# Performance work log

Measured on AMD Instinct MI355X. Metric: run time of the kernel, lower is better.

## Reference

```python
import jax, jax.numpy as jnp
import numpy as np
from jax import lax

S, B, IN, H, L = 256, 8192, 1, 32, 2


def setup_inputs() -> dict:
    key = jax.random.key(0)
    ks = jax.random.split(key, 12)
    s = 1.0 / np.sqrt(H)
    return {
        "x": jax.random.normal(ks[0], (S, B, IN), dtype=jnp.float32),
        "h": jax.random.normal(ks[1], (L, B, H), dtype=jnp.float32),
        "W_ih0": jax.random.uniform(ks[2], (3 * H, IN), jnp.float32, -s, s),
        "W_hh0": jax.random.uniform(ks[3], (3 * H, H), jnp.float32, -s, s),
        "b_ih0": jax.random.uniform(ks[4], (3 * H,), jnp.float32, -s, s),
        "b_hh0": jax.random.uniform(ks[5], (3 * H,), jnp.float32, -s, s),
        "W_ih1": jax.random.uniform(ks[6], (3 * H, H), jnp.float32, -s, s),
        "W_hh1": jax.random.uniform(ks[7], (3 * H, H), jnp.float32, -s, s),
        "b_ih1": jax.random.uniform(ks[8], (3 * H,), jnp.float32, -s, s),
        "b_hh1": jax.random.uniform(ks[9], (3 * H,), jnp.float32, -s, s),
        "W_out": jax.random.uniform(ks[10], (1, H), jnp.float32, -s, s),
        "b_out": jax.random.uniform(ks[11], (1,), jnp.float32, -s, s),
    }


def _gru_layer(x_seq, h0, W_ih, W_hh, b_ih, b_hh):
    # x_seq: (S, B, D_in), h0: (B, H). PyTorch GRU gate math.
    def step(h, x_t):
        gi = x_t @ W_ih.T + b_ih            # (B, 3H)
        gh = h @ W_hh.T + b_hh              # (B, 3H)
        i_r, i_z, i_n = jnp.split(gi, 3, axis=-1)
        h_r, h_z, h_n = jnp.split(gh, 3, axis=-1)
        r = jax.nn.sigmoid(i_r + h_r)
        z = jax.nn.sigmoid(i_z + h_z)
        n = jnp.tanh(i_n + r * h_n)
        h_new = (1.0 - z) * n + z * h
        return h_new, h_new

    h_last, out = lax.scan(step, h0, x_seq)
    return out, h_last


def reference(x, h, W_ih0, W_hh0, b_ih0, b_hh0, W_ih1, W_hh1, b_ih1, b_hh1, W_out, b_out):
    out0, hl0 = _gru_layer(x, h[0], W_ih0, W_hh0, b_ih0, b_hh0)
    out1, hl1 = _gru_layer(out0, h[1], W_ih1, W_hh1, b_ih1, b_hh1)
    # per-timestep Linear loop == one batched matmul over (S, B, H)
    y = out1 @ W_out.T + b_out              # (S, B, 1)
    h_state = jnp.stack([hl0, hl1], axis=0)  # (L, B, H)
    return (y, h_state)
```

## Files before the change

kernel.cpp:

```cpp
#include <hip/hip_runtime.h>


#define S_LEN 256
#define B_SZ  8192
#define H_SZ  32
#define RS    40

typedef __attribute__((ext_vector_type(8))) short short8;
typedef __attribute__((ext_vector_type(4))) float f32x4;

#define MFMA(a, b, c) __builtin_amdgcn_mfma_f32_16x16x32_bf16(a, b, c, 0, 0, 0)

#if __has_builtin(__builtin_amdgcn_exp2f)
#define EXP2F(x) __builtin_amdgcn_exp2f(x)
#else
#define EXP2F(x) exp2f(x)
#endif
#if __has_builtin(__builtin_amdgcn_rcpf)
#define RCPF(x) __builtin_amdgcn_rcpf(x)
#else
#define RCPF(x) (1.0f / (x))
#endif

__device__ __forceinline__ float sigm_pre(float p) {
    return RCPF(1.0f + EXP2F(p));
}
__device__ __forceinline__ float tanh_pre(float p) {
    return 1.0f - 2.0f * RCPF(1.0f + EXP2F(p));
}

__device__ __forceinline__ unsigned short bf_rne1(float f) {
    union { float f; unsigned u; } x; x.f = f;
    unsigned u = x.u + 0x7fffu + ((x.u >> 16) & 1u);
    return (unsigned short)(u >> 16);
}

#if __has_builtin(__builtin_amdgcn_cvt_pk_bf16_f32)
typedef __bf16 bf16x2 __attribute__((ext_vector_type(2)));
__device__ __forceinline__ unsigned pk2(float a, float b) {
    union { bf16x2 v; unsigned u; } c;
    c.v = __builtin_amdgcn_cvt_pk_bf16_f32(a, b);
    return c.u;
}
#else
__device__ __forceinline__ unsigned pk2(float a, float b) {
    return (unsigned)bf_rne1(a) | ((unsigned)bf_rne1(b) << 16);
}
#endif

union Frag { short8 s8; unsigned u[4]; };

__global__ __launch_bounds__(256) void gru_bf(
    const float* __restrict__ x,
    const float* __restrict__ h_in,
    const float* __restrict__ W_ih0,
    const float* __restrict__ W_hh0,
    const float* __restrict__ b_ih0,
    const float* __restrict__ b_hh0,
    const float* __restrict__ W_ih1,
    const float* __restrict__ W_hh1,
    const float* __restrict__ b_ih1,
    const float* __restrict__ b_hh1,
    const float* __restrict__ W_out,
    const float* __restrict__ b_out,
    float* __restrict__ out)
{
    __shared__ __align__(16) float sx[S_LEN * 16];
    __shared__ __align__(16) float sy[2][S_LEN * 16];
    __shared__ __align__(16) unsigned short sh0s[3][16 * RS];
    __shared__ __align__(16) unsigned short sh1s[3][16 * RS];

    const int tid  = threadIdx.x;
    const int w    = tid >> 6;
    const int lane = tid & 63;
    const int n    = lane & 15;
    const int q    = lane >> 4;
    const int base = blockIdx.x * 16;
    const int bn   = base + n;
    const int wl   = w & 1;

    for (int s = tid; s < S_LEN * 4; s += 256) {
        const int t = s >> 2, c = s & 3;
        *(float4*)&sx[t * 16 + c * 4] = *(const float4*)&x[t * B_SZ + base + c * 4];
    }

    const float SRZ = -1.4426950408889634f;
    const float SN  =  2.8853900817779268f;

    short8 A_h[3], A_i[3];
    f32x4  C_h[3], C_i3;
    float  wi0r[4], wi0z[4], wi0n[4], bi0n[4];
    float  wo[4];
    float  hd[4];

    if (w < 2) {
#pragma unroll
        for (int t = 0; t < 3; ++t) {
            const float sc = (t < 2) ? SRZ : SN;
            const int row = 32 * t + 16 * wl + n;
#pragma unroll
            for (int e = 0; e < 8; ++e)
                A_h[t][e] = (short)bf_rne1(W_hh0[row * H_SZ + q * 8 + e] * sc);
#pragma unroll
            for (int r = 0; r < 4; ++r) {
                const int g = 32 * t + 16 * wl + 4 * q + r;
                C_h[t][r] = (t < 2) ? SRZ * (b_ih0[g] + b_hh0[g])
                                    : SN * b_hh0[g];
            }
        }
#pragma unroll
        for (int r = 0; r < 4; ++r) {
            const int j = 16 * wl + 4 * q + r;
            wi0r[r] = SRZ * W_ih0[j];
            wi0z[r] = SRZ * W_ih0[32 + j];
            wi0n[r] = SN  * W_ih0[64 + j];
            bi0n[r] = SN  * b_ih0[64 + j];
            hd[r]   = h_in[bn * H_SZ + j];
            wo[r]   = 0.f;
        }
    } else {
#pragma unroll
        for (int t = 0; t < 3; ++t) {
            const float sc = (t < 2) ? SRZ : SN;
            const int row = 32 * t + 16 * wl + n;
#pragma unroll
            for (int e = 0; e < 8; ++e) {
                A_h[t][e] = (short)bf_rne1(W_hh1[row * H_SZ + q * 8 + e] * sc);
                A_i[t][e] = (short)bf_rne1(W_ih1[row * H_SZ + q * 8 + e] * sc);
            }
#pragma unroll
            for (int r = 0; r < 4; ++r) {
                const int g = 32 * t + 16 * wl + 4 * q + r;
                C_h[t][r] = (t < 2) ? SRZ * (b_ih1[g] + b_hh1[g])
                                    : SN * b_hh1[g];
                if (t == 2) C_i3[r] = SN * b_ih1[g];
            }
        }
#pragma unroll
        for (int r = 0; r < 4; ++r) {
            const int j = 16 * wl + 4 * q + r;
            hd[r] = h_in[B_SZ * H_SZ + bn * H_SZ + j];
            wo[r] = W_out[j];
        }
    }
    const f32x4 Z4 = {0.f, 0.f, 0.f, 0.f};
    const float bout = b_out[0];

    short8 B0, B1;
    {
        Frag f;
        const float4 a = *(const float4*)&h_in[bn * H_SZ + q * 8];
        const float4 b = *(const float4*)&h_in[bn * H_SZ + q * 8 + 4];
        f.u[0] = pk2(a.x, a.y); f.u[1] = pk2(a.z, a.w);
        f.u[2] = pk2(b.x, b.y); f.u[3] = pk2(b.z, b.w);
        B0 = f.s8;
        const float4 c = *(const float4*)&h_in[B_SZ * H_SZ + bn * H_SZ + q * 8];
        const float4 d = *(const float4*)&h_in[B_SZ * H_SZ + bn * H_SZ + q * 8 + 4];
        f.u[0] = pk2(c.x, c.y); f.u[1] = pk2(c.z, c.w);
        f.u[2] = pk2(d.x, d.y); f.u[3] = pk2(d.z, d.w);
        B1 = f.s8;
    }

    __syncthreads();

    int buf = 0;
#pragma unroll 1
    for (int i = 0; i <= S_LEN; ++i) {
        if (w < 2) {
            if (i < S_LEN) {
                const float xc = sx[i * 16 + n];
                const f32x4 g0r = MFMA(A_h[0], B0, C_h[0]);
                const f32x4 g0z = MFMA(A_h[1], B0, C_h[1]);
                const f32x4 g0n = MFMA(A_h[2], B0, C_h[2]);
                float hv4[4];
#pragma unroll
                for (int r = 0; r < 4; ++r) {
                    const float rg = sigm_pre(fmaf(xc, wi0r[r], g0r[r]));
                    const float zg = sigm_pre(fmaf(xc, wi0z[r], g0z[r]));
                    const float ng = tanh_pre(fmaf(rg, g0n[r],
                                                   fmaf(xc, wi0n[r], bi0n[r])));
                    const float hv = fmaf(zg, hd[r] - ng, ng);
                    hd[r] = hv;
                    hv4[r] = hv;
                }
                *(uint2*)&sh0s[buf][n * RS + 16 * wl + 4 * q] =
                    make_uint2(pk2(hv4[0], hv4[1]), pk2(hv4[2], hv4[3]));
            }
        } else {
            if (i > 0) {
                const f32x4 ur = MFMA(A_h[0], B1, C_h[0]);
                const f32x4 uz = MFMA(A_h[1], B1, C_h[1]);
                const f32x4 un = MFMA(A_h[2], B1, C_h[2]);
                const f32x4 vr = MFMA(A_i[0], B0, Z4);
                const f32x4 vz = MFMA(A_i[1], B0, Z4);
                const f32x4 vn = MFMA(A_i[2], B0, C_i3);
                float hv4[4];
                float ys = 0.f;
#pragma unroll
                for (int r = 0; r < 4; ++r) {
                    const float rg = sigm_pre(ur[r] + vr[r]);
                    const float zg = sigm_pre(uz[r] + vz[r]);
                    const float ng = tanh_pre(fmaf(rg, un[r], vn[r]));
                    const float hv = fmaf(zg, hd[r] - ng, ng);
                    hd[r] = hv;
                    hv4[r] = hv;
                    ys = fmaf(hv, wo[r], ys);
                }
                *(uint2*)&sh1s[buf][n * RS + 16 * wl + 4 * q] =
                    make_uint2(pk2(hv4[0], hv4[1]), pk2(hv4[2], hv4[3]));
                ys += __shfl_xor(ys, 16);
                ys += __shfl_xor(ys, 32);
                if (lane < 16) sy[wl][(i - 1) * 16 + n] = ys;
            }
        }

        __syncthreads();

        if (i < S_LEN)
            B0 = *(const short8*)&sh0s[buf][n * RS + q * 8];
        if (w >= 2 && i > 0)
            B1 = *(const short8*)&sh1s[buf][n * RS + q * 8];

        buf = (buf == 2) ? 0 : buf + 1;
    }

    __syncthreads();

    for (int s = tid; s < S_LEN * 4; s += 256) {
        const int t = s >> 2, c = s & 3;
        const float4 a = *(const float4*)&sy[0][t * 16 + c * 4];
        const float4 b = *(const float4*)&sy[1][t * 16 + c * 4];
        *(float4*)&out[t * B_SZ + base + c * 4] =
            make_float4(a.x + b.x + bout, a.y + b.y + bout,
                        a.z + b.z + bout, a.w + b.w + bout);
    }

    const int j = 16 * wl + 4 * q;
    if (w < 2)
        *(float4*)&out[S_LEN * B_SZ + bn * H_SZ + j] =
            make_float4(hd[0], hd[1], hd[2], hd[3]);
    else
        *(float4*)&out[S_LEN * B_SZ + B_SZ * H_SZ + bn * H_SZ + j] =
            make_float4(hd[0], hd[1], hd[2], hd[3]);
}

extern "C" void kernel_launch(void* const* d_in, const int* in_sizes, int n_in,
                              void* d_out, int out_size, void* d_ws, size_t ws_size,
                              hipStream_t stream) {
    (void)in_sizes; (void)n_in; (void)out_size; (void)d_ws; (void)ws_size;
    const float* x     = (const float*)d_in[0];
    const float* h_in  = (const float*)d_in[1];
    const float* W_ih0 = (const float*)d_in[2];
    const float* W_hh0 = (const float*)d_in[3];
    const float* b_ih0 = (const float*)d_in[4];
    const float* b_hh0 = (const float*)d_in[5];
    const float* W_ih1 = (const float*)d_in[6];
    const float* W_hh1 = (const float*)d_in[7];
    const float* b_ih1 = (const float*)d_in[8];
    const float* b_hh1 = (const float*)d_in[9];
    const float* W_out = (const float*)d_in[10];
    const float* b_out = (const float*)d_in[11];

    dim3 grid(B_SZ / 16);
    dim3 block(256);
    gru_bf<<<grid, block, 0, stream>>>(x, h_in, W_ih0, W_hh0, b_ih0, b_hh0,
                                       W_ih1, W_hh1, b_ih1, b_hh1,
                                       W_out, b_out, (float*)d_out);
}
```

Baseline: 269.0 us.

## Process two 16-column batch groups per wave for ILP in the GRU recurrence

Each block now handles 32 batch columns, and every wave runs two independent 16-column groups through the MFMA and gate math. This halves the grid and interleaves two dependency chains to hide MFMA and transcendental latency in the serial time loop. The output projection moves from the layer-1 waves to the otherwise lighter layer-0 waves, read back from shared memory, and the hidden-state ring buffer drops from three slots to two. x is now stored as bf16 in shared memory, which adds rounding error on the layer-0 input. Register pressure also rises with doubled accumulators and state.

```diff
diff --git a/kernel.cpp b/kernel.cpp
--- a/kernel.cpp
+++ b/kernel.cpp
@@ -48,9 +48,11 @@
 }
 #endif
 
-union Frag { short8 s8; unsigned u[4]; };
-
-__global__ __launch_bounds__(256) void gru_bf(
+__device__ __forceinline__ float bits_f(unsigned u) {
+    union { unsigned u; float f; } x; x.u = u; return x.f;
+}
+
+__global__ __launch_bounds__(256) void gru_ilp2(
     const float* __restrict__ x,
     const float* __restrict__ h_in,
     const float* __restrict__ W_ih0,
@@ -65,23 +67,24 @@
     const float* __restrict__ b_out,
     float* __restrict__ out)
 {
-    __shared__ __align__(16) float sx[S_LEN * 16];
-    __shared__ __align__(16) float sy[2][S_LEN * 16];
-    __shared__ __align__(16) unsigned short sh0s[3][16 * RS];
-    __shared__ __align__(16) unsigned short sh1s[3][16 * RS];
+    __shared__ __align__(16) unsigned short sxs[S_LEN * 32];
+    __shared__ __align__(16) float sy[S_LEN * 32];
+    __shared__ __align__(16) unsigned short sh0s[2][32 * RS];
+    __shared__ __align__(16) unsigned short sh1s[2][32 * RS];
 
     const int tid  = threadIdx.x;
     const int w    = tid >> 6;
     const int lane = tid & 63;
     const int n    = lane & 15;
     const int q    = lane >> 4;
-    const int base = blockIdx.x * 16;
-    const int bn   = base + n;
+    const int base = blockIdx.x * 32;
     const int wl   = w & 1;
 
-    for (int s = tid; s < S_LEN * 4; s += 256) {
-        const int t = s >> 2, c = s & 3;
-        *(float4*)&sx[t * 16 + c * 4] = *(const float4*)&x[t * B_SZ + base + c * 4];
+    for (int s = tid; s < S_LEN * 8; s += 256) {
+        const int t = s >> 3, c = s & 7;
+        const float4 v = *(const float4*)&x[t * B_SZ + base + c * 4];
+        *(uint2*)&sxs[t * 32 + c * 4] =
+            make_uint2(pk2(v.x, v.y), pk2(v.z, v.w));
     }
 
     const float SRZ = -1.4426950408889634f;
@@ -90,8 +93,8 @@
     short8 A_h[3], A_i[3];
     f32x4  C_h[3], C_i3;
     float  wi0r[4], wi0z[4], wi0n[4], bi0n[4];
-    float  wo[4];
-    float  hd[4];
+    float  wo8[8];
+    float  hd[2][4];
 
     if (w < 2) {
 #pragma unroll
@@ -115,9 +118,14 @@
             wi0z[r] = SRZ * W_ih0[32 + j];
             wi0n[r] = SN  * W_ih0[64 + j];
             bi0n[r] = SN  * b_ih0[64 + j];
-            hd[r]   = h_in[bn * H_SZ + j];
-            wo[r]   = 0.f;
-        }
+        }
+#pragma unroll
+        for (int e = 0; e < 8; ++e) wo8[e] = W_out[q * 8 + e];
+#pragma unroll
+        for (int g = 0; g < 2; ++g)
+#pragma unroll
+            for (int r = 0; r < 4; ++r)
+                hd[g][r] = h_in[(base + g * 16 + n) * H_SZ + 16 * wl + 4 * q + r];
     } else {
 #pragma unroll
         for (int t = 0; t < 3; ++t) {
@@ -137,111 +145,150 @@
             }
         }
 #pragma unroll
-        for (int r = 0; r < 4; ++r) {
-            const int j = 16 * wl + 4 * q + r;
-            hd[r] = h_in[B_SZ * H_SZ + bn * H_SZ + j];
-            wo[r] = W_out[j];
-        }
+        for (int g = 0; g < 2; ++g)
+#pragma unroll
+            for (int r = 0; r < 4; ++r)
+                hd[g][r] = h_in[B_SZ * H_SZ +
+                                (base + g * 16 + n) * H_SZ + 16 * wl + 4 * q + r];
     }
     const f32x4 Z4 = {0.f, 0.f, 0.f, 0.f};
     const float bout = b_out[0];
 
-    short8 B0, B1;
-    {
-        Frag f;
-        const float4 a = *(const float4*)&h_in[bn * H_SZ + q * 8];
-        const float4 b = *(const float4*)&h_in[bn * H_SZ + q * 8 + 4];
+    short8 B0[2], B1[2];
+#pragma unroll
+    for (int g = 0; g < 2; ++g) {
+        const int bg = base + g * 16 + n;
+        union { short8 s8; unsigned u[4]; } f;
+        float4 a = *(const float4*)&h_in[bg * H_SZ + q * 8];
+        float4 b = *(const float4*)&h_in[bg * H_SZ + q * 8 + 4];
         f.u[0] = pk2(a.x, a.y); f.u[1] = pk2(a.z, a.w);
         f.u[2] = pk2(b.x, b.y); f.u[3] = pk2(b.z, b.w);
-        B0 = f.s8;
-        const float4 c = *(const float4*)&h_in[B_SZ * H_SZ + bn * H_SZ + q * 8];
-        const float4 d = *(const float4*)&h_in[B_SZ * H_SZ + bn * H_SZ + q * 8 + 4];
-        f.u[0] = pk2(c.x, c.y); f.u[1] = pk2(c.z, c.w);
-        f.u[2] = pk2(d.x, d.y); f.u[3] = pk2(d.z, d.w);
-        B1 = f.s8;
+        B0[g] = f.s8;
+        a = *(const float4*)&h_in[B_SZ * H_SZ + bg * H_SZ + q * 8];
+        b = *(const float4*)&h_in[B_SZ * H_SZ + bg * H_SZ + q * 8 + 4];
+        f.u[0] = pk2(a.x, a.y); f.u[1] = pk2(a.z, a.w);
+        f.u[2] = pk2(b.x, b.y); f.u[3] = pk2(b.z, b.w);
+        B1[g] = f.s8;
     }
 
     __syncthreads();
 
-    int buf = 0;
 #pragma unroll 1
     for (int i = 0; i <= S_LEN; ++i) {
+        const int buf = i & 1;
         if (w < 2) {
             if (i < S_LEN) {
-                const float xc = sx[i * 16 + n];
-                const f32x4 g0r = MFMA(A_h[0], B0, C_h[0]);
-                const f32x4 g0z = MFMA(A_h[1], B0, C_h[1]);
-                const f32x4 g0n = MFMA(A_h[2], B0, C_h[2]);
-                float hv4[4];
-#pragma unroll
-                for (int r = 0; r < 4; ++r) {
-                    const float rg = sigm_pre(fmaf(xc, wi0r[r], g0r[r]));
-                    const float zg = sigm_pre(fmaf(xc, wi0z[r], g0z[r]));
-                    const float ng = tanh_pre(fmaf(rg, g0n[r],
-                                                   fmaf(xc, wi0n[r], bi0n[r])));
-                    const float hv = fmaf(zg, hd[r] - ng, ng);
-                    hd[r] = hv;
-                    hv4[r] = hv;
+                const f32x4 g0r = MFMA(A_h[0], B0[0], C_h[0]);
+                const f32x4 g0z = MFMA(A_h[1], B0[0], C_h[1]);
+                const f32x4 g0n = MFMA(A_h[2], B0[0], C_h[2]);
+                const f32x4 g1r = MFMA(A_h[0], B0[1], C_h[0]);
+                const f32x4 g1z = MFMA(A_h[1], B0[1], C_h[1]);
+                const f32x4 g1n = MFMA(A_h[2], B0[1], C_h[2]);
+                const float xc0 = bits_f((unsigned)sxs[i * 32 + n] << 16);
+                const float xc1 = bits_f((unsigned)sxs[i * 32 + 16 + n] << 16);
+#pragma unroll
+                for (int g = 0; g < 2; ++g) {
+                    const float xc = g ? xc1 : xc0;
+                    float hv4[4];
+#pragma unroll
+                    for (int r = 0; r < 4; ++r) {
+                        const float gr = g ? g1r[r] : g0r[r];
+                        const float gz = g ? g1z[r] : g0z[r];
+                        const float gn = g ? g1n[r] : g0n[r];
+                        const float rg = sigm_pre(fmaf(xc, wi0r[r], gr));
+                        const float zg = sigm_pre(fmaf(xc, wi0z[r], gz));
+                        const float ng = tanh_pre(fmaf(rg, gn,
+                                                       fmaf(xc, wi0n[r], bi0n[r])));
+                        const float hv = fmaf(zg, hd[g][r] - ng, ng);
+                        hd[g][r] = hv;
+                        hv4[r] = hv;
+                    }
+                    *(uint2*)&sh0s[buf][(g * 16 + n) * RS + 16 * wl + 4 * q] =
+                        make_uint2(pk2(hv4[0], hv4[1]), pk2(hv4[2], hv4[3]));
                 }
-                *(uint2*)&sh0s[buf][n * RS + 16 * wl + 4 * q] =
-                    make_uint2(pk2(hv4[0], hv4[1]), pk2(hv4[2], hv4[3]));
             }
         } else {
             if (i > 0) {
-                const f32x4 ur = MFMA(A_h[0], B1, C_h[0]);
-                const f32x4 uz = MFMA(A_h[1], B1, C_h[1]);
-                const f32x4 un = MFMA(A_h[2], B1, C_h[2]);
-                const f32x4 vr = MFMA(A_i[0], B0, Z4);
-                const f32x4 vz = MFMA(A_i[1], B0, Z4);
-                const f32x4 vn = MFMA(A_i[2], B0, C_i3);
-                float hv4[4];
-                float ys = 0.f;
-#pragma unroll
-                for (int r = 0; r < 4; ++r) {
-                    const float rg = sigm_pre(ur[r] + vr[r]);
-                    const float zg = sigm_pre(uz[r] + vz[r]);
-                    const float ng = tanh_pre(fmaf(rg, un[r], vn[r]));
-                    const float hv = fmaf(zg, hd[r] - ng, ng);
-                    hd[r] = hv;
-                    hv4[r] = hv;
-                    ys = fmaf(hv, wo[r], ys);
+                const f32x4 u0r = MFMA(A_h[0], B1[0], C_h[0]);
+                const f32x4 u0z = MFMA(A_h[1], B1[0], C_h[1]);
+                const f32x4 u0n = MFMA(A_h[2], B1[0], C_h[2]);
+                const f32x4 v0r = MFMA(A_i[0], B0[0], Z4);
+                const f32x4 v0z = MFMA(A_i[1], B0[0], Z4);
+                const f32x4 v0n = MFMA(A_i[2], B0[0], C_i3);
+                const f32x4 u1r = MFMA(A_h[0], B1[1], C_h[0]);
+                const f32x4 u1z = MFMA(A_h[1], B1[1], C_h[1]);
+                const f32x4 u1n = MFMA(A_h[2], B1[1], C_h[2]);
+                const f32x4 v1r = MFMA(A_i[0], B0[1], Z4);
+                const f32x4 v1z = MFMA(A_i[1], B0[1], Z4);
+                const f32x4 v1n = MFMA(A_i[2], B0[1], C_i3);
+#pragma unroll
+                for (int g = 0; g < 2; ++g) {
+                    float hv4[4];
+#pragma unroll
+                    for (int r = 0; r < 4; ++r) {
+                        const float ar = g ? u1r[r] + v1r[r] : u0r[r] + v0r[r];
+                        const float az = g ? u1z[r] + v1z[r] : u0z[r] + v0z[r];
+                        const float an = g ? u1n[r] : u0n[r];
+                        const float bn_ = g ? v1n[r] : v0n[r];
+                        const float rg = sigm_pre(ar);
+                        const float zg = sigm_pre(az);
+                        const float ng = tanh_pre(fmaf(rg, an, bn_));
+                        const float hv = fmaf(zg, hd[g][r] - ng, ng);
+                        hd[g][r] = hv;
+                        hv4[r] = hv;
+                    }
+                    *(uint2*)&sh1s[buf][(g * 16 + n) * RS + 16 * wl + 4 * q] =
+                        make_uint2(pk2(hv4[0], hv4[1]), pk2(hv4[2], hv4[3]));
                 }
-                *(uint2*)&sh1s[buf][n * RS + 16 * wl + 4 * q] =
-                    make_uint2(pk2(hv4[0], hv4[1]), pk2(hv4[2], hv4[3]));
-                ys += __shfl_xor(ys, 16);
-                ys += __shfl_xor(ys, 32);
-                if (lane < 16) sy[wl][(i - 1) * 16 + n] = ys;
             }
         }
 
         __syncthreads();
 
-        if (i < S_LEN)
-            B0 = *(const short8*)&sh0s[buf][n * RS + q * 8];
-        if (w >= 2 && i > 0)
-            B1 = *(const short8*)&sh1s[buf][n * RS + q * 8];
-
-        buf = (buf == 2) ? 0 : buf + 1;
+        if (i < S_LEN) {
+            B0[0] = *(const short8*)&sh0s[buf][n * RS + q * 8];
+            B0[1] = *(const short8*)&sh0s[buf][(16 + n) * RS + q * 8];
+            if (w >= 2 && i > 0) {
+                B1[0] = *(const short8*)&sh1s[buf][n * RS + q * 8];
+                B1[1] = *(const short8*)&sh1s[buf][(16 + n) * RS + q * 8];
+            }
+        }
+        if (w < 2 && i > 0) {
+            const uint4 d = *(const uint4*)&sh1s[buf][(wl * 16 + n) * RS + q * 8];
+            float ys =       bits_f(d.x << 16) * wo8[0];
+            ys = fmaf(bits_f(d.x & 0xffff0000u), wo8[1], ys);
+            ys = fmaf(bits_f(d.y << 16),         wo8[2], ys);
+            ys = fmaf(bits_f(d.y & 0xffff0000u), wo8[3], ys);
+            ys = fmaf(bits_f(d.z << 16),         wo8[4], ys);
+            ys = fmaf(bits_f(d.z & 0xffff0000u), wo8[5], ys);
+            ys = fmaf(bits_f(d.w << 16),         wo8[6], ys);
+            ys = fmaf(bits_f(d.w & 0xffff0000u), wo8[7], ys);
+            ys += __shfl_xor(ys, 16);
+            ys += __shfl_xor(ys, 32);
+            if (lane < 16) sy[(i - 1) * 32 + wl * 16 + n] = ys;
+        }
     }
 
     __syncthreads();
 
-    for (int s = tid; s < S_LEN * 4; s += 256) {
-        const int t = s >> 2, c = s & 3;
-        const float4 a = *(const float4*)&sy[0][t * 16 + c * 4];
-        const float4 b = *(const float4*)&sy[1][t * 16 + c * 4];
+    for (int s = tid; s < S_LEN * 8; s += 256) {
+        const int t = s >> 3, c = s & 7;
+        const float4 a = *(const float4*)&sy[t * 32 + c * 4];
         *(float4*)&out[t * B_SZ + base + c * 4] =
-            make_float4(a.x + b.x + bout, a.y + b.y + bout,
-                        a.z + b.z + bout, a.w + b.w + bout);
+            make_float4(a.x + bout, a.y + bout, a.z + bout, a.w + bout);
     }
 
     const int j = 16 * wl + 4 * q;
-    if (w < 2)
-        *(float4*)&out[S_LEN * B_SZ + bn * H_SZ + j] =
-            make_float4(hd[0], hd[1], hd[2], hd[3]);
-    else
-        *(float4*)&out[S_LEN * B_SZ + B_SZ * H_SZ + bn * H_SZ + j] =
-            make_float4(hd[0], hd[1], hd[2], hd[3]);
+#pragma unroll
+    for (int g = 0; g < 2; ++g) {
+        const int bg = base + g * 16 + n;
+        if (w < 2)
+            *(float4*)&out[S_LEN * B_SZ + bg * H_SZ + j] =
+                make_float4(hd[g][0], hd[g][1], hd[g][2], hd[g][3]);
+        else
+            *(float4*)&out[S_LEN * B_SZ + B_SZ * H_SZ + bg * H_SZ + j] =
+                make_float4(hd[g][0], hd[g][1], hd[g][2], hd[g][3]);
+    }
 }
 
 extern "C" void kernel_launch(void* const* d_in, const int* in_sizes, int n_in,
@@ -261,9 +308,9 @@
     const float* W_out = (const float*)d_in[10];
     const float* b_out = (const float*)d_in[11];
 
-    dim3 grid(B_SZ / 16);
+    dim3 grid(B_SZ / 32);
     dim3 block(256);
-    gru_bf<<<grid, block, 0, stream>>>(x, h_in, W_ih0, W_hh0, b_ih0, b_hh0,
-                                       W_ih1, W_hh1, b_ih1, b_hh1,
-                                       W_out, b_out, (float*)d_out);
-}
+    gru_ilp2<<<grid, block, 0, stream>>>(x, h_in, W_ih0, W_hh0, b_ih0, b_hh0,
+                                         W_ih1, W_hh1, b_ih1, b_hh1,
+                                         W_out, b_out, (float*)d_out);
+}
```

Result: slower. 289.7 us (+7.7%).

## Give each GRU layer a single wave and pipeline layers through an LDS ring

Applied to the files above, without the earlier changes.

Each layer's whole 32-wide hidden state now lives in one wavefront, so the per-step recurrence needs no block barrier. Layer 0 runs ahead in segments of 8 timesteps and writes its hidden states into a 16-slot LDS ring. Layer 1 consumes the previous segment and does its own recurrence through a private LDS transpose buffer, which cuts block-wide barriers from one per step to one per segment. The cost is twice the MFMA and activation work per wave, fewer waves per block (128 threads), and serialized latency inside each wave.

```diff
diff --git a/kernel.cpp b/kernel.cpp
--- a/kernel.cpp
+++ b/kernel.cpp
@@ -5,6 +5,8 @@
 #define B_SZ  8192
 #define H_SZ  32
 #define RS    40
+#define SEG   8
+#define NSLOT 16
 
 typedef __attribute__((ext_vector_type(8))) short short8;
 typedef __attribute__((ext_vector_type(4))) float f32x4;
@@ -48,9 +50,7 @@
 }
 #endif
 
-union Frag { short8 s8; unsigned u[4]; };
-
-__global__ __launch_bounds__(256) void gru_bf(
+__global__ __launch_bounds__(128, 1) void gru_auto(
     const float* __restrict__ x,
     const float* __restrict__ h_in,
     const float* __restrict__ W_ih0,
@@ -65,10 +65,10 @@
     const float* __restrict__ b_out,
     float* __restrict__ out)
 {
+    __shared__ __align__(16) unsigned short ring[NSLOT][16 * RS];
+    __shared__ __align__(16) unsigned short tr1[16 * RS];
     __shared__ __align__(16) float sx[S_LEN * 16];
-    __shared__ __align__(16) float sy[2][S_LEN * 16];
-    __shared__ __align__(16) unsigned short sh0s[3][16 * RS];
-    __shared__ __align__(16) unsigned short sh1s[3][16 * RS];
+    __shared__ __align__(16) float sy[S_LEN * 16];
 
     const int tid  = threadIdx.x;
     const int w    = tid >> 6;
@@ -77,9 +77,8 @@
     const int q    = lane >> 4;
     const int base = blockIdx.x * 16;
     const int bn   = base + n;
-    const int wl   = w & 1;
-
-    for (int s = tid; s < S_LEN * 4; s += 256) {
+
+    for (int s = tid; s < S_LEN * 4; s += 128) {
         const int t = s >> 2, c = s & 3;
         *(float4*)&sx[t * 16 + c * 4] = *(const float4*)&x[t * B_SZ + base + c * 4];
     }
@@ -87,161 +86,175 @@
     const float SRZ = -1.4426950408889634f;
     const float SN  =  2.8853900817779268f;
 
-    short8 A_h[3], A_i[3];
-    f32x4  C_h[3], C_i3;
-    float  wi0r[4], wi0z[4], wi0n[4], bi0n[4];
-    float  wo[4];
-    float  hd[4];
-
-    if (w < 2) {
-#pragma unroll
-        for (int t = 0; t < 3; ++t) {
-            const float sc = (t < 2) ? SRZ : SN;
-            const int row = 32 * t + 16 * wl + n;
+    short8 Am[6], Aa[6];
+    f32x4  Cm[6], Ca[2];
+    float  wir[2][4], wiz[2][4], win[2][4], bin[2][4];
+    float  wo[2][4];
+    float  hd[2][4];
+    short8 B0, B1, B0n;
+
+    if (w == 0) {
+#pragma unroll
+        for (int T = 0; T < 6; ++T) {
+            const float sc = (T < 4) ? SRZ : SN;
+            const int row = 16 * T + n;
 #pragma unroll
             for (int e = 0; e < 8; ++e)
-                A_h[t][e] = (short)bf_rne1(W_hh0[row * H_SZ + q * 8 + e] * sc);
-#pragma unroll
-            for (int r = 0; r < 4; ++r) {
-                const int g = 32 * t + 16 * wl + 4 * q + r;
-                C_h[t][r] = (t < 2) ? SRZ * (b_ih0[g] + b_hh0[g])
-                                    : SN * b_hh0[g];
+                Am[T][e] = (short)bf_rne1(W_hh0[row * H_SZ + q * 8 + e] * sc);
+#pragma unroll
+            for (int r = 0; r < 4; ++r) {
+                const int g = 16 * T + 4 * q + r;
+                Cm[T][r] = (T < 4) ? SRZ * (b_ih0[g] + b_hh0[g])
+                                   : SN * b_hh0[g];
             }
         }
 #pragma unroll
-        for (int r = 0; r < 4; ++r) {
-            const int j = 16 * wl + 4 * q + r;
-            wi0r[r] = SRZ * W_ih0[j];
-            wi0z[r] = SRZ * W_ih0[32 + j];
-            wi0n[r] = SN  * W_ih0[64 + j];
-            bi0n[r] = SN  * b_ih0[64 + j];
-            hd[r]   = h_in[bn * H_SZ + j];
-            wo[r]   = 0.f;
-        }
-    } else {
-#pragma unroll
-        for (int t = 0; t < 3; ++t) {
-            const float sc = (t < 2) ? SRZ : SN;
-            const int row = 32 * t + 16 * wl + n;
-#pragma unroll
-            for (int e = 0; e < 8; ++e) {
-                A_h[t][e] = (short)bf_rne1(W_hh1[row * H_SZ + q * 8 + e] * sc);
-                A_i[t][e] = (short)bf_rne1(W_ih1[row * H_SZ + q * 8 + e] * sc);
-            }
-#pragma unroll
-            for (int r = 0; r < 4; ++r) {
-                const int g = 32 * t + 16 * wl + 4 * q + r;
-                C_h[t][r] = (t < 2) ? SRZ * (b_ih1[g] + b_hh1[g])
-                                    : SN * b_hh1[g];
-                if (t == 2) C_i3[r] = SN * b_ih1[g];
-            }
-        }
-#pragma unroll
-        for (int r = 0; r < 4; ++r) {
-            const int j = 16 * wl + 4 * q + r;
-            hd[r] = h_in[B_SZ * H_SZ + bn * H_SZ + j];
-            wo[r] = W_out[j];
-        }
-    }
-    const f32x4 Z4 = {0.f, 0.f, 0.f, 0.f};
-    const float bout = b_out[0];
-
-    short8 B0, B1;
-    {
-        Frag f;
+        for (int h = 0; h < 2; ++h)
+#pragma unroll
+            for (int r = 0; r < 4; ++r) {
+                const int j = 16 * h + 4 * q + r;
+                wir[h][r] = SRZ * W_ih0[j];
+                wiz[h][r] = SRZ * W_ih0[32 + j];
+                win[h][r] = SN  * W_ih0[64 + j];
+                bin[h][r] = SN  * b_ih0[64 + j];
+                hd[h][r]  = h_in[bn * H_SZ + j];
+            }
+        union { short8 s8; unsigned u[4]; } f;
         const float4 a = *(const float4*)&h_in[bn * H_SZ + q * 8];
         const float4 b = *(const float4*)&h_in[bn * H_SZ + q * 8 + 4];
         f.u[0] = pk2(a.x, a.y); f.u[1] = pk2(a.z, a.w);
         f.u[2] = pk2(b.x, b.y); f.u[3] = pk2(b.z, b.w);
         B0 = f.s8;
-        const float4 c = *(const float4*)&h_in[B_SZ * H_SZ + bn * H_SZ + q * 8];
-        const float4 d = *(const float4*)&h_in[B_SZ * H_SZ + bn * H_SZ + q * 8 + 4];
-        f.u[0] = pk2(c.x, c.y); f.u[1] = pk2(c.z, c.w);
-        f.u[2] = pk2(d.x, d.y); f.u[3] = pk2(d.z, d.w);
+    } else {
+#pragma unroll
+        for (int T = 0; T < 6; ++T) {
+            const float sc = (T < 4) ? SRZ : SN;
+            const int row = 16 * T + n;
+#pragma unroll
+            for (int e = 0; e < 8; ++e) {
+                Am[T][e] = (short)bf_rne1(W_hh1[row * H_SZ + q * 8 + e] * sc);
+                Aa[T][e] = (short)bf_rne1(W_ih1[row * H_SZ + q * 8 + e] * sc);
+            }
+#pragma unroll
+            for (int r = 0; r < 4; ++r) {
+                const int g = 16 * T + 4 * q + r;
+                Cm[T][r] = (T < 4) ? SRZ * (b_ih1[g] + b_hh1[g])
+                                   : SN * b_hh1[g];
+                if (T >= 4) Ca[T - 4][r] = SN * b_ih1[g];
+            }
+        }
+#pragma unroll
+        for (int h = 0; h < 2; ++h)
+#pragma unroll
+            for (int r = 0; r < 4; ++r) {
+                const int j = 16 * h + 4 * q + r;
+                hd[h][r] = h_in[B_SZ * H_SZ + bn * H_SZ + j];
+                wo[h][r] = W_out[j];
+            }
+        union { short8 s8; unsigned u[4]; } f;
+        const float4 a = *(const float4*)&h_in[B_SZ * H_SZ + bn * H_SZ + q * 8];
+        const float4 b = *(const float4*)&h_in[B_SZ * H_SZ + bn * H_SZ + q * 8 + 4];
+        f.u[0] = pk2(a.x, a.y); f.u[1] = pk2(a.z, a.w);
+        f.u[2] = pk2(b.x, b.y); f.u[3] = pk2(b.z, b.w);
         B1 = f.s8;
     }
+    const f32x4 Z4 = {0.f, 0.f, 0.f, 0.f};
+    const float bout = b_out[0];
+
+    const int lsr  = n * RS + 8 * q;
+    const int lsw0 = n * RS + 4 * q;
+    const int lsw1 = n * RS + 16 + 4 * q;
 
     __syncthreads();
 
-    int buf = 0;
 #pragma unroll 1
-    for (int i = 0; i <= S_LEN; ++i) {
-        if (w < 2) {
-            if (i < S_LEN) {
-                const float xc = sx[i * 16 + n];
-                const f32x4 g0r = MFMA(A_h[0], B0, C_h[0]);
-                const f32x4 g0z = MFMA(A_h[1], B0, C_h[1]);
-                const f32x4 g0n = MFMA(A_h[2], B0, C_h[2]);
-                float hv4[4];
-#pragma unroll
-                for (int r = 0; r < 4; ++r) {
-                    const float rg = sigm_pre(fmaf(xc, wi0r[r], g0r[r]));
-                    const float zg = sigm_pre(fmaf(xc, wi0z[r], g0z[r]));
-                    const float ng = tanh_pre(fmaf(rg, g0n[r],
-                                                   fmaf(xc, wi0n[r], bi0n[r])));
-                    const float hv = fmaf(zg, hd[r] - ng, ng);
-                    hd[r] = hv;
-                    hv4[r] = hv;
+    for (int m = 0; m <= S_LEN / SEG; ++m) {
+        if (w == 0) {
+            if (m < S_LEN / SEG) {
+#pragma unroll 1
+                for (int k = 0; k < SEG; ++k) {
+                    const int t = m * SEG + k;
+                    f32x4 D[6];
+#pragma unroll
+                    for (int T = 0; T < 6; ++T) D[T] = MFMA(Am[T], B0, Cm[T]);
+                    const float xc = sx[t * 16 + n];
+                    unsigned short* slot = &ring[t & (NSLOT - 1)][0];
+                    float hv[2][4];
+#pragma unroll
+                    for (int h = 0; h < 2; ++h)
+#pragma unroll
+                        for (int r = 0; r < 4; ++r) {
+                            const float rg = sigm_pre(fmaf(xc, wir[h][r], D[h][r]));
+                            const float zg = sigm_pre(fmaf(xc, wiz[h][r], D[2 + h][r]));
+                            const float ng = tanh_pre(fmaf(rg, D[4 + h][r],
+                                                           fmaf(xc, win[h][r], bin[h][r])));
+                            const float v = fmaf(zg, hd[h][r] - ng, ng);
+                            hd[h][r] = v;
+                            hv[h][r] = v;
+                        }
+                    *(uint2*)&slot[lsw0] =
+                        make_uint2(pk2(hv[0][0], hv[0][1]), pk2(hv[0][2], hv[0][3]));
+                    *(uint2*)&slot[lsw1] =
+                        make_uint2(pk2(hv[1][0], hv[1][1]), pk2(hv[1][2], hv[1][3]));
+                    B0 = *(const short8*)&slot[lsr];
                 }
-                *(uint2*)&sh0s[buf][n * RS + 16 * wl + 4 * q] =
-                    make_uint2(pk2(hv4[0], hv4[1]), pk2(hv4[2], hv4[3]));
             }
         } else {
-            if (i > 0) {
-                const f32x4 ur = MFMA(A_h[0], B1, C_h[0]);
-                const f32x4 uz = MFMA(A_h[1], B1, C_h[1]);
-                const f32x4 un = MFMA(A_h[2], B1, C_h[2]);
-                const f32x4 vr = MFMA(A_i[0], B0, Z4);
-                const f32x4 vz = MFMA(A_i[1], B0, Z4);
-                const f32x4 vn = MFMA(A_i[2], B0, C_i3);
-                float hv4[4];
-                float ys = 0.f;
-#pragma unroll
-                for (int r = 0; r < 4; ++r) {
-                    const float rg = sigm_pre(ur[r] + vr[r]);
-                    const float zg = sigm_pre(uz[r] + vz[r]);
-                    const float ng = tanh_pre(fmaf(rg, un[r], vn[r]));
-                    const float hv = fmaf(zg, hd[r] - ng, ng);
-                    hd[r] = hv;
-                    hv4[r] = hv;
-                    ys = fmaf(hv, wo[r], ys);
+            if (m > 0) {
+                const int t0 = (m - 1) * SEG;
+                B0 = *(const short8*)&ring[t0 & (NSLOT - 1)][lsr];
+#pragma unroll 1
+                for (int k = 0; k < SEG; ++k) {
+                    const int t = t0 + k;
+                    f32x4 U[6], V[6];
+#pragma unroll
+                    for (int T = 0; T < 6; ++T) U[T] = MFMA(Am[T], B1, Cm[T]);
+#pragma unroll
+                    for (int T = 0; T < 6; ++T)
+                        V[T] = MFMA(Aa[T], B0, (T >= 4) ? Ca[T - 4] : Z4);
+                    if (k + 1 < SEG)
+                        B0n = *(const short8*)&ring[(t + 1) & (NSLOT - 1)][lsr];
+                    float hv[2][4];
+                    float ys = 0.f;
+#pragma unroll
+                    for (int h = 0; h < 2; ++h)
+#pragma unroll
+                        for (int r = 0; r < 4; ++r) {
+                            const float rg = sigm_pre(U[h][r] + V[h][r]);
+                            const float zg = sigm_pre(U[2 + h][r] + V[2 + h][r]);
+                            const float ng = tanh_pre(fmaf(rg, U[4 + h][r], V[4 + h][r]));
+                            const float v = fmaf(zg, hd[h][r] - ng, ng);
+                            hd[h][r] = v;
+                            hv[h][r] = v;
+                            ys = fmaf(v, wo[h][r], ys);
+                        }
+                    *(uint2*)&tr1[lsw0] =
+                        make_uint2(pk2(hv[0][0], hv[0][1]), pk2(hv[0][2], hv[0][3]));
+                    *(uint2*)&tr1[lsw1] =
+                        make_uint2(pk2(hv[1][0], hv[1][1]), pk2(hv[1][2], hv[1][3]));
+                    B1 = *(const short8*)&tr1[lsr];
+                    ys += __shfl_xor(ys, 16);
+                    ys += __shfl_xor(ys, 32);
+                    if (lane < 16) sy[t * 16 + n] = ys;
+                    B0 = B0n;
                 }
-                *(uint2*)&sh1s[buf][n * RS + 16 * wl + 4 * q] =
-                    make_uint2(pk2(hv4[0], hv4[1]), pk2(hv4[2], hv4[3]));
-                ys += __shfl_xor(ys, 16);
-                ys += __shfl_xor(ys, 32);
-                if (lane < 16) sy[wl][(i - 1) * 16 + n] = ys;
             }
         }
-
         __syncthreads();
-
-        if (i < S_LEN)
-            B0 = *(const short8*)&sh0s[buf][n * RS + q * 8];
-        if (w >= 2 && i > 0)
-            B1 = *(const short8*)&sh1s[buf][n * RS + q * 8];
-
-        buf = (buf == 2) ? 0 : buf + 1;
-    }
-
-    __syncthreads();
-
-    for (int s = tid; s < S_LEN * 4; s += 256) {
+    }
+
+    for (int s = tid; s < S_LEN * 4; s += 128) {
         const int t = s >> 2, c = s & 3;
-        const float4 a = *(const float4*)&sy[0][t * 16 + c * 4];
-        const float4 b = *(const float4*)&sy[1][t * 16 + c * 4];
+        const float4 a = *(const float4*)&sy[t * 16 + c * 4];
         *(float4*)&out[t * B_SZ + base + c * 4] =
-            make_float4(a.x + b.x + bout, a.y + b.y + bout,
-                        a.z + b.z + bout, a.w + b.w + bout);
-    }
-
-    const int j = 16 * wl + 4 * q;
-    if (w < 2)
-        *(float4*)&out[S_LEN * B_SZ + bn * H_SZ + j] =
-            make_float4(hd[0], hd[1], hd[2], hd[3]);
-    else
-        *(float4*)&out[S_LEN * B_SZ + B_SZ * H_SZ + bn * H_SZ + j] =
-            make_float4(hd[0], hd[1], hd[2], hd[3]);
+            make_float4(a.x + bout, a.y + bout, a.z + bout, a.w + bout);
+    }
+
+    const size_t hoff = (size_t)S_LEN * B_SZ + (size_t)(w == 1) * B_SZ * H_SZ;
+#pragma unroll
+    for (int h = 0; h < 2; ++h)
+        *(float4*)&out[hoff + bn * H_SZ + 16 * h + 4 * q] =
+            make_float4(hd[h][0], hd[h][1], hd[h][2], hd[h][3]);
 }
 
 extern "C" void kernel_launch(void* const* d_in, const int* in_sizes, int n_in,
@@ -262,8 +275,8 @@
     const float* b_out = (const float*)d_in[11];
 
     dim3 grid(B_SZ / 16);
-    dim3 block(256);
-    gru_bf<<<grid, block, 0, stream>>>(x, h_in, W_ih0, W_hh0, b_ih0, b_hh0,
-                                       W_ih1, W_hh1, b_ih1, b_hh1,
-                                       W_out, b_out, (float*)d_out);
-}
+    dim3 block(128);
+    gru_auto<<<grid, block, 0, stream>>>(x, h_in, W_ih0, W_hh0, b_ih0, b_hh0,
+                                         W_ih1, W_hh1, b_ih1, b_hh1,
+                                         W_out, b_out, (float*)d_out);
+}
```

After: 373.2 us. 1.39x slower.

## Split GRU gate epilogue across twice the waves per block

Applied to the files above, without the earlier changes.

Doubles the block to 512 threads (8 waves). Each pair of waves now computes the same three MFMAs redundantly but each handles only two of the four output rows, which halves the per-wave transcendental epilogue on the serial recurrence critical path. The output projection moves to a single layer-1 wave that works from the bf16 hidden state read back from shared memory, so the sy buffer shrinks to one copy. The cost is duplicated MFMA work and more waves joining each per-step barrier, and y is now computed from bf16-rounded hidden states.

```diff
diff --git a/kernel.cpp b/kernel.cpp
--- a/kernel.cpp
+++ b/kernel.cpp
@@ -48,9 +48,11 @@
 }
 #endif
 
-union Frag { short8 s8; unsigned u[4]; };
-
-__global__ __launch_bounds__(256) void gru_bf(
+__device__ __forceinline__ float bits_f(unsigned u) {
+    union { unsigned u; float f; } x; x.u = u; return x.f;
+}
+
+__global__ __launch_bounds__(512, 4) void gru_rsplit(
     const float* __restrict__ x,
     const float* __restrict__ h_in,
     const float* __restrict__ W_ih0,
@@ -65,21 +67,23 @@
     const float* __restrict__ b_out,
     float* __restrict__ out)
 {
+    __shared__ __align__(16) unsigned short sh0[3][16 * RS];
+    __shared__ __align__(16) unsigned short sh1[3][16 * RS];
     __shared__ __align__(16) float sx[S_LEN * 16];
-    __shared__ __align__(16) float sy[2][S_LEN * 16];
-    __shared__ __align__(16) unsigned short sh0s[3][16 * RS];
-    __shared__ __align__(16) unsigned short sh1s[3][16 * RS];
-
-    const int tid  = threadIdx.x;
-    const int w    = tid >> 6;
-    const int lane = tid & 63;
-    const int n    = lane & 15;
-    const int q    = lane >> 4;
-    const int base = blockIdx.x * 16;
-    const int bn   = base + n;
-    const int wl   = w & 1;
-
-    for (int s = tid; s < S_LEN * 4; s += 256) {
+    __shared__ __align__(16) float sy[S_LEN * 16];
+
+    const int tid   = threadIdx.x;
+    const int w     = tid >> 6;
+    const int lane  = tid & 63;
+    const int n     = lane & 15;
+    const int q     = lane >> 4;
+    const int layer = w >> 2;
+    const int hl    = (w >> 1) & 1;
+    const int rp    = w & 1;
+    const int base  = blockIdx.x * 16;
+    const int bn    = base + n;
+
+    for (int s = tid; s < S_LEN * 4; s += 512) {
         const int t = s >> 2, c = s & 3;
         *(float4*)&sx[t * 16 + c * 4] = *(const float4*)&x[t * B_SZ + base + c * 4];
     }
@@ -87,161 +91,167 @@
     const float SRZ = -1.4426950408889634f;
     const float SN  =  2.8853900817779268f;
 
-    short8 A_h[3], A_i[3];
-    f32x4  C_h[3], C_i3;
-    float  wi0r[4], wi0z[4], wi0n[4], bi0n[4];
-    float  wo[4];
-    float  hd[4];
-
-    if (w < 2) {
-#pragma unroll
-        for (int t = 0; t < 3; ++t) {
-            const float sc = (t < 2) ? SRZ : SN;
-            const int row = 32 * t + 16 * wl + n;
-#pragma unroll
-            for (int e = 0; e < 8; ++e)
-                A_h[t][e] = (short)bf_rne1(W_hh0[row * H_SZ + q * 8 + e] * sc);
-#pragma unroll
-            for (int r = 0; r < 4; ++r) {
-                const int g = 32 * t + 16 * wl + 4 * q + r;
-                C_h[t][r] = (t < 2) ? SRZ * (b_ih0[g] + b_hh0[g])
-                                    : SN * b_hh0[g];
+    const float* Wm = layer ? W_hh1 : W_hh0;
+    const float* bi = layer ? b_ih1 : b_ih0;
+    const float* bh = layer ? b_hh1 : b_hh0;
+
+    short8 Ar, Az, An, Pr, Pz, Pn;
+    f32x4  Cr, Cz, Cn, Ci;
+    {
+        const int rowr = 16 * hl + n;
+        const int rowz = 32 + 16 * hl + n;
+        const int rown = 64 + 16 * hl + n;
+#pragma unroll
+        for (int e = 0; e < 8; ++e) {
+            Ar[e] = (short)bf_rne1(Wm[rowr * H_SZ + q * 8 + e] * SRZ);
+            Az[e] = (short)bf_rne1(Wm[rowz * H_SZ + q * 8 + e] * SRZ);
+            An[e] = (short)bf_rne1(Wm[rown * H_SZ + q * 8 + e] * SN);
+        }
+        if (layer) {
+#pragma unroll
+            for (int e = 0; e < 8; ++e) {
+                Pr[e] = (short)bf_rne1(W_ih1[rowr * H_SZ + q * 8 + e] * SRZ);
+                Pz[e] = (short)bf_rne1(W_ih1[rowz * H_SZ + q * 8 + e] * SRZ);
+                Pn[e] = (short)bf_rne1(W_ih1[rown * H_SZ + q * 8 + e] * SN);
             }
         }
 #pragma unroll
         for (int r = 0; r < 4; ++r) {
-            const int j = 16 * wl + 4 * q + r;
-            wi0r[r] = SRZ * W_ih0[j];
-            wi0z[r] = SRZ * W_ih0[32 + j];
-            wi0n[r] = SN  * W_ih0[64 + j];
-            bi0n[r] = SN  * b_ih0[64 + j];
-            hd[r]   = h_in[bn * H_SZ + j];
-            wo[r]   = 0.f;
-        }
-    } else {
-#pragma unroll
-        for (int t = 0; t < 3; ++t) {
-            const float sc = (t < 2) ? SRZ : SN;
-            const int row = 32 * t + 16 * wl + n;
-#pragma unroll
-            for (int e = 0; e < 8; ++e) {
-                A_h[t][e] = (short)bf_rne1(W_hh1[row * H_SZ + q * 8 + e] * sc);
-                A_i[t][e] = (short)bf_rne1(W_ih1[row * H_SZ + q * 8 + e] * sc);
-            }
-#pragma unroll
-            for (int r = 0; r < 4; ++r) {
-                const int g = 32 * t + 16 * wl + 4 * q + r;
-                C_h[t][r] = (t < 2) ? SRZ * (b_ih1[g] + b_hh1[g])
-                                    : SN * b_hh1[g];
-                if (t == 2) C_i3[r] = SN * b_ih1[g];
-            }
-        }
-#pragma unroll
-        for (int r = 0; r < 4; ++r) {
-            const int j = 16 * wl + 4 * q + r;
-            hd[r] = h_in[B_SZ * H_SZ + bn * H_SZ + j];
-            wo[r] = W_out[j];
-        }
+            const int g = 16 * hl + 4 * q + r;
+            Cr[r] = SRZ * (bi[g] + bh[g]);
+            Cz[r] = SRZ * (bi[32 + g] + bh[32 + g]);
+            Cn[r] = SN * bh[64 + g];
+            Ci[r] = SN * bi[64 + g];
+        }
+    }
+    float wir[2], wiz[2], win[2], bin[2];
+    if (!layer) {
+#pragma unroll
+        for (int s = 0; s < 2; ++s) {
+            const int j = 16 * hl + 4 * q + 2 * rp + s;
+            wir[s] = SRZ * W_ih0[j];
+            wiz[s] = SRZ * W_ih0[32 + j];
+            win[s] = SN  * W_ih0[64 + j];
+            bin[s] = SN  * b_ih0[64 + j];
+        }
+    }
+    float wo8[8];
+    if (w == 4) {
+#pragma unroll
+        for (int e = 0; e < 8; ++e) wo8[e] = W_out[q * 8 + e];
     }
     const f32x4 Z4 = {0.f, 0.f, 0.f, 0.f};
     const float bout = b_out[0];
 
+    float hd[2];
+    {
+        const float* hsrc = h_in + (size_t)layer * B_SZ * H_SZ + bn * H_SZ;
+        hd[0] = hsrc[16 * hl + 4 * q + 2 * rp];
+        hd[1] = hsrc[16 * hl + 4 * q + 2 * rp + 1];
+    }
     short8 B0, B1;
     {
-        Frag f;
-        const float4 a = *(const float4*)&h_in[bn * H_SZ + q * 8];
-        const float4 b = *(const float4*)&h_in[bn * H_SZ + q * 8 + 4];
+        const float* hsrc = h_in + (size_t)layer * B_SZ * H_SZ + bn * H_SZ + q * 8;
+        union { short8 s8; unsigned u[4]; } f;
+        const float4 a = *(const float4*)&hsrc[0];
+        const float4 b = *(const float4*)&hsrc[4];
         f.u[0] = pk2(a.x, a.y); f.u[1] = pk2(a.z, a.w);
         f.u[2] = pk2(b.x, b.y); f.u[3] = pk2(b.z, b.w);
-        B0 = f.s8;
-        const float4 c = *(const float4*)&h_in[B_SZ * H_SZ + bn * H_SZ + q * 8];
-        const float4 d = *(const float4*)&h_in[B_SZ * H_SZ + bn * H_SZ + q * 8 + 4];
-        f.u[0] = pk2(c.x, c.y); f.u[1] = pk2(c.z, c.w);
-        f.u[2] = pk2(d.x, d.y); f.u[3] = pk2(d.z, d.w);
-        B1 = f.s8;
-    }
+        if (layer) B1 = f.s8; else B0 = f.s8;
+    }
+
+    const int wroff = n * RS + 16 * hl + 4 * q + 2 * rp;
+    const int rdoff = n * RS + 8 * q;
 
     __syncthreads();
 
-    int buf = 0;
+    int bw = 0;
 #pragma unroll 1
     for (int i = 0; i <= S_LEN; ++i) {
-        if (w < 2) {
+        if (layer == 0) {
             if (i < S_LEN) {
+                const f32x4 Dr = MFMA(Ar, B0, Cr);
+                const f32x4 Dz = MFMA(Az, B0, Cz);
+                const f32x4 Dn = MFMA(An, B0, Cn);
                 const float xc = sx[i * 16 + n];
-                const f32x4 g0r = MFMA(A_h[0], B0, C_h[0]);
-                const f32x4 g0z = MFMA(A_h[1], B0, C_h[1]);
-                const f32x4 g0n = MFMA(A_h[2], B0, C_h[2]);
-                float hv4[4];
-#pragma unroll
-                for (int r = 0; r < 4; ++r) {
-                    const float rg = sigm_pre(fmaf(xc, wi0r[r], g0r[r]));
-                    const float zg = sigm_pre(fmaf(xc, wi0z[r], g0z[r]));
-                    const float ng = tanh_pre(fmaf(rg, g0n[r],
-                                                   fmaf(xc, wi0n[r], bi0n[r])));
-                    const float hv = fmaf(zg, hd[r] - ng, ng);
-                    hd[r] = hv;
-                    hv4[r] = hv;
+                float hv0, hv1;
+#pragma unroll
+                for (int s = 0; s < 2; ++s) {
+                    const int rr = 2 * rp + s;
+                    const float rg = sigm_pre(fmaf(xc, wir[s], Dr[rr]));
+                    const float zg = sigm_pre(fmaf(xc, wiz[s], Dz[rr]));
+                    const float ng = tanh_pre(fmaf(rg, Dn[rr],
+                                                   fmaf(xc, win[s], bin[s])));
+                    const float v = fmaf(zg, hd[s] - ng, ng);
+                    hd[s] = v;
+                    if (s == 0) hv0 = v; else hv1 = v;
                 }
-                *(uint2*)&sh0s[buf][n * RS + 16 * wl + 4 * q] =
-                    make_uint2(pk2(hv4[0], hv4[1]), pk2(hv4[2], hv4[3]));
+                *(unsigned*)&sh0[bw][wroff] = pk2(hv0, hv1);
             }
         } else {
             if (i > 0) {
-                const f32x4 ur = MFMA(A_h[0], B1, C_h[0]);
-                const f32x4 uz = MFMA(A_h[1], B1, C_h[1]);
-                const f32x4 un = MFMA(A_h[2], B1, C_h[2]);
-                const f32x4 vr = MFMA(A_i[0], B0, Z4);
-                const f32x4 vz = MFMA(A_i[1], B0, Z4);
-                const f32x4 vn = MFMA(A_i[2], B0, C_i3);
-                float hv4[4];
-                float ys = 0.f;
-#pragma unroll
-                for (int r = 0; r < 4; ++r) {
-                    const float rg = sigm_pre(ur[r] + vr[r]);
-                    const float zg = sigm_pre(uz[r] + vz[r]);
-                    const float ng = tanh_pre(fmaf(rg, un[r], vn[r]));
-                    const float hv = fmaf(zg, hd[r] - ng, ng);
-                    hd[r] = hv;
-                    hv4[r] = hv;
-                    ys = fmaf(hv, wo[r], ys);
+                const f32x4 Ur = MFMA(Ar, B1, Cr);
+                const f32x4 Uz = MFMA(Az, B1, Cz);
+                const f32x4 Un = MFMA(An, B1, Cn);
+                const f32x4 Vr = MFMA(Pr, B0, Z4);
+                const f32x4 Vz = MFMA(Pz, B0, Z4);
+                const f32x4 Vn = MFMA(Pn, B0, Ci);
+                float hv0, hv1;
+#pragma unroll
+                for (int s = 0; s < 2; ++s) {
+                    const int rr = 2 * rp + s;
+                    const float rg = sigm_pre(Ur[rr] + Vr[rr]);
+                    const float zg = sigm_pre(Uz[rr] + Vz[rr]);
+                    const float ng = tanh_pre(fmaf(rg, Un[rr], Vn[rr]));
+                    const float v = fmaf(zg, hd[s] - ng, ng);
+                    hd[s] = v;
+                    if (s == 0) hv0 = v; else hv1 = v;
                 }
-                *(uint2*)&sh1s[buf][n * RS + 16 * wl + 4 * q] =
-                    make_uint2(pk2(hv4[0], hv4[1]), pk2(hv4[2], hv4[3]));
-                ys += __shfl_xor(ys, 16);
-                ys += __shfl_xor(ys, 32);
-                if (lane < 16) sy[wl][(i - 1) * 16 + n] = ys;
+                *(unsigned*)&sh1[bw][wroff] = pk2(hv0, hv1);
             }
         }
 
         __syncthreads();
 
-        if (i < S_LEN)
-            B0 = *(const short8*)&sh0s[buf][n * RS + q * 8];
-        if (w >= 2 && i > 0)
-            B1 = *(const short8*)&sh1s[buf][n * RS + q * 8];
-
-        buf = (buf == 2) ? 0 : buf + 1;
+        if (layer == 0) {
+            if (i < S_LEN)
+                B0 = *(const short8*)&sh0[bw][rdoff];
+        } else {
+            if (i < S_LEN)
+                B0 = *(const short8*)&sh0[bw][rdoff];
+            if (i > 0) {
+                B1 = *(const short8*)&sh1[bw][rdoff];
+                if (w == 4) {
+                    union { short8 s8; unsigned u[4]; } f; f.s8 = B1;
+                    float ys = bits_f(f.u[0] << 16) * wo8[0];
+                    ys = fmaf(bits_f(f.u[0] & 0xffff0000u), wo8[1], ys);
+                    ys = fmaf(bits_f(f.u[1] << 16),         wo8[2], ys);
+                    ys = fmaf(bits_f(f.u[1] & 0xffff0000u), wo8[3], ys);
+                    ys = fmaf(bits_f(f.u[2] << 16),         wo8[4], ys);
+                    ys = fmaf(bits_f(f.u[2] & 0xffff0000u), wo8[5], ys);
+                    ys = fmaf(bits_f(f.u[3] << 16),         wo8[6], ys);
+                    ys = fmaf(bits_f(f.u[3] & 0xffff0000u), wo8[7], ys);
+                    ys += __shfl_xor(ys, 16);
+                    ys += __shfl_xor(ys, 32);
+                    if (lane < 16) sy[(i - 1) * 16 + n] = ys;
+                }
+            }
+        }
+        bw = (bw == 2) ? 0 : bw + 1;
     }
 
     __syncthreads();
 
-    for (int s = tid; s < S_LEN * 4; s += 256) {
+    for (int s = tid; s < S_LEN * 4; s += 512) {
         const int t = s >> 2, c = s & 3;
-        const float4 a = *(const float4*)&sy[0][t * 16 + c * 4];
-        const float4 b = *(const float4*)&sy[1][t * 16 + c * 4];
+        const float4 a = *(const float4*)&sy[t * 16 + c * 4];
         *(float4*)&out[t * B_SZ + base + c * 4] =
-            make_float4(a.x + b.x + bout, a.y + b.y + bout,
-                        a.z + b.z + bout, a.w + b.w + bout);
-    }
-
-    const int j = 16 * wl + 4 * q;
-    if (w < 2)
-        *(float4*)&out[S_LEN * B_SZ + bn * H_SZ + j] =
-            make_float4(hd[0], hd[1], hd[2], hd[3]);
-    else
-        *(float4*)&out[S_LEN * B_SZ + B_SZ * H_SZ + bn * H_SZ + j] =
-            make_float4(hd[0], hd[1], hd[2], hd[3]);
+            make_float4(a.x + bout, a.y + bout, a.z + bout, a.w + bout);
+    }
+
+    const size_t hoff = (size_t)S_LEN * B_SZ + (size_t)layer * B_SZ * H_SZ;
+    *(float2*)&out[hoff + bn * H_SZ + 16 * hl + 4 * q + 2 * rp] =
+        make_float2(hd[0], hd[1]);
 }
 
 extern "C" void kernel_launch(void* const* d_in, const int* in_sizes, int n_in,
@@ -262,8 +272,8 @@
     const float* b_out = (const float*)d_in[11];
 
     dim3 grid(B_SZ / 16);
-    dim3 block(256);
-    gru_bf<<<grid, block, 0, stream>>>(x, h_in, W_ih0, W_hh0, b_ih0, b_hh0,
-                                       W_ih1, W_hh1, b_ih1, b_hh1,
-                                       W_out, b_out, (float*)d_out);
-}
+    dim3 block(512);
+    gru_rsplit<<<grid, block, 0, stream>>>(x, h_in, W_ih0, W_hh0, b_ih0, b_hh0,
+                                           W_ih1, W_hh1, b_ih1, b_hh1,
+                                           W_out, b_out, (float*)d_out);
+}
```

After: 317.5 us. +18.1%, slower.
